# Kernel tuning notes

Hardware: AMD Instinct MI355X
Metric: run time of the kernel (lower is better)

The kernel has to match this reference:

```python
import jax, jax.numpy as jnp
import numpy as np

N_NODES = 100000
N_EDGES = 640000
F_DIM = 128   # node_feature_dim
D_DIM = 128   # state_dim
ROUNDS = 4


def setup_inputs() -> dict:
    key = jax.random.key(0)
    ks = jax.random.split(key, 8)
    s = 1.0 / np.sqrt(D_DIM)
    return {
        "x": jax.random.normal(ks[0], (N_NODES, F_DIM), dtype=jnp.float32),
        "edge_index": jax.random.randint(ks[1], (2, N_EDGES), 0, N_NODES, dtype=jnp.int64),
        "Wi": jax.random.normal(ks[2], (F_DIM, D_DIM), dtype=jnp.float32) * s,
        "bi": jax.random.normal(ks[3], (D_DIM,), dtype=jnp.float32) * s,
        "Wm": jax.random.normal(ks[4], (ROUNDS, D_DIM, D_DIM), dtype=jnp.float32) * s,
        "bm": jax.random.normal(ks[5], (ROUNDS, D_DIM), dtype=jnp.float32) * s,
        "Wu": jax.random.normal(ks[6], (ROUNDS, D_DIM, D_DIM), dtype=jnp.float32) * s,
        "bu": jax.random.normal(ks[7], (ROUNDS, D_DIM), dtype=jnp.float32) * s,
    }


def reference(x, edge_index, Wi, bi, Wm, bm, Wu, bu):
    num_nodes = x.shape[0]
    src = edge_index[0]  # from-node (messages are gathered from here)
    dst = edge_index[1]  # to-node (scatter-add target)

    # input_net: Linear + ReLU
    state = jax.nn.relu(x @ Wi + bi)  # (N, D)

    def step(state, params):
        Wm_r, bm_r, Wu_r, bu_r = params
        message = jax.nn.relu(state @ Wm_r + bm_r)          # (N, D)
        gathered = message[src]                              # (E, D) gather
        aggregated = jax.ops.segment_sum(gathered, dst,
                                         num_segments=num_nodes)  # scatter-add
        return state + jax.nn.relu(aggregated @ Wu_r + bu_r), None

    state, _ = jax.lax.scan(step, state, (Wm, bm, Wu, bu))
    # original: zeros(state_dim) + state broadcasts to (N, D)
    return state
```

## Files before the change

### kernel.cpp

```cpp
#include <hip/hip_runtime.h>

#define NN 100000
#define NE 640000
#define DD 128
#define ROUNDS 4
#define CAP 32
#define NFT 3125
#define GEMMB 512
#define KPH 136

typedef float f32x4 __attribute__((ext_vector_type(4)));
typedef _Float16 half8 __attribute__((ext_vector_type(8)));

__global__ __launch_bounds__(128) void wprep_k(
    const float* __restrict__ Wi, const float* __restrict__ Wm,
    const float* __restrict__ Wu, _Float16* __restrict__ WT)
{
    const int mat = blockIdx.x >> 7;
    const int k   = blockIdx.x & 127;
    const int n   = threadIdx.x;
    const float* W = (mat == 0) ? Wi
                   : (mat <= 4) ? Wm + (size_t)(mat - 1) * DD * DD
                                : Wu + (size_t)(mat - 5) * DD * DD;
    WT[(size_t)mat * DD * DD + (size_t)n * DD + k] = (_Float16)W[(size_t)k * DD + n];
}

__global__ __launch_bounds__(256, 2) void prep_k(
    const float* __restrict__ x,
    const _Float16* __restrict__ WiT, const _Float16* __restrict__ Wm0T,
    const float* __restrict__ bi, const float* __restrict__ bm0,
    _Float16* __restrict__ Sh, _Float16* __restrict__ msg0,
    const int* __restrict__ src, const int* __restrict__ dst,
    int* __restrict__ cursor, int* __restrict__ bucket)
{
    for (int e = blockIdx.x * 256 + threadIdx.x; e < NE; e += GEMMB * 256) {
        const int d = dst[e];
        const int s = src[e];
        const int pos = atomicAdd(&cursor[d], 1);
        if (pos < CAP) bucket[(long long)d * CAP + pos] = s;
    }

    __shared__ _Float16 Ash[32 * KPH];

    const int tid  = threadIdx.x;
    const int lane = tid & 63;
    const int wave = tid >> 6;
    const int ln   = lane & 15;
    const int q    = lane >> 4;
    const int st   = (wave & 1) * 16;
    const int colBase = (wave >> 1) * 64;

    half8 WI[4][4], WM[4][4];
#pragma unroll
    for (int s = 0; s < 4; s++) {
#pragma unroll
        for (int b = 0; b < 4; b++) {
            const size_t off = (size_t)(colBase + b * 16 + ln) * DD + s * 32 + q * 8;
            WI[s][b] = *(const half8*)&WiT[off];
            WM[s][b] = *(const half8*)&Wm0T[off];
        }
    }
    float biasi[4], biasm[4];
#pragma unroll
    for (int b = 0; b < 4; b++) {
        biasi[b] = bi[colBase + b * 16 + ln];
        biasm[b] = bm0[colBase + b * 16 + ln];
    }

    for (int tileB = blockIdx.x; tileB < NFT; tileB += GEMMB) {
        const float* p = x + ((size_t)tileB * 32 + st + ln) * DD + q * 8;
        half8 xa[4];
#pragma unroll
        for (int s = 0; s < 4; s++) {
            const float4 f0 = *(const float4*)&p[s * 32];
            const float4 f1 = *(const float4*)&p[s * 32 + 4];
            half8 h;
            h[0] = (_Float16)f0.x; h[1] = (_Float16)f0.y;
            h[2] = (_Float16)f0.z; h[3] = (_Float16)f0.w;
            h[4] = (_Float16)f1.x; h[5] = (_Float16)f1.y;
            h[6] = (_Float16)f1.z; h[7] = (_Float16)f1.w;
            xa[s] = h;
        }

        f32x4 acc[4];
#pragma unroll
        for (int b = 0; b < 4; b++)
            acc[b] = (f32x4){biasi[b], biasi[b], biasi[b], biasi[b]};
#pragma unroll
        for (int s = 0; s < 4; s++)
#pragma unroll
            for (int b = 0; b < 4; b++)
                acc[b] = __builtin_amdgcn_mfma_f32_16x16x32_f16(xa[s], WI[s][b], acc[b], 0, 0, 0);

        __syncthreads();
#pragma unroll
        for (int b = 0; b < 4; b++) {
            const int col = colBase + b * 16 + ln;
#pragma unroll
            for (int r = 0; r < 4; r++) {
                const size_t row = (size_t)tileB * 32 + st + q * 4 + r;
                const _Float16 v = (_Float16)fmaxf(acc[b][r], 0.f);
                Sh[row * DD + col] = v;
                Ash[(st + q * 4 + r) * KPH + col] = v;
            }
        }
        __syncthreads();

        f32x4 acc2[4];
#pragma unroll
        for (int b = 0; b < 4; b++)
            acc2[b] = (f32x4){biasm[b], biasm[b], biasm[b], biasm[b]};
#pragma unroll
        for (int s = 0; s < 4; s++) {
            const half8 aS = *(const half8*)&Ash[(st + ln) * KPH + s * 32 + q * 8];
#pragma unroll
            for (int b = 0; b < 4; b++)
                acc2[b] = __builtin_amdgcn_mfma_f32_16x16x32_f16(aS, WM[s][b], acc2[b], 0, 0, 0);
        }
#pragma unroll
        for (int b = 0; b < 4; b++) {
            const int col = colBase + b * 16 + ln;
#pragma unroll
            for (int r = 0; r < 4; r++) {
                const size_t row = (size_t)tileB * 32 + st + q * 4 + r;
                msg0[row * DD + col] = (_Float16)fmaxf(acc2[b][r], 0.f);
            }
        }
    }
}

__global__ __launch_bounds__(256, 2) void fused_round_k(
    const _Float16* __restrict__ msgIn,
    const int* __restrict__ cursor,
    const int* __restrict__ bucket,
    const _Float16* __restrict__ WuT, const float* __restrict__ bu_r,
    const _Float16* __restrict__ WmT, const float* __restrict__ bm_r,
    const _Float16* __restrict__ Rh,
    _Float16* __restrict__ ShOut,
    _Float16* __restrict__ msgOut,
    float* __restrict__ Of)
{
    __shared__ _Float16 Ash[32 * KPH];

    const int tid  = threadIdx.x;
    const int lane = tid & 63;
    const int wave = tid >> 6;
    const int ln   = lane & 15;
    const int q    = lane >> 4;
    const int st   = (wave & 1) * 16;
    const int colBase = (wave >> 1) * 64;

    half8 WU[4][4], WM[4][4];
#pragma unroll
    for (int s = 0; s < 4; s++) {
#pragma unroll
        for (int b = 0; b < 4; b++) {
            const size_t off = (size_t)(colBase + b * 16 + ln) * DD + s * 32 + q * 8;
            WU[s][b] = *(const half8*)&WuT[off];
            if (WmT) WM[s][b] = *(const half8*)&WmT[off];
        }
    }
    float biasu[4], biasm[4];
#pragma unroll
    for (int b = 0; b < 4; b++) {
        biasu[b] = bu_r[colBase + b * 16 + ln];
        biasm[b] = WmT ? bm_r[colBase + b * 16 + ln] : 0.f;
    }

    const int grow = tid >> 3;
    const int grp  = tid & 7;
    const int gcol = grp * 16;

    int cnt = 0;
    int idxr[4];
#pragma unroll
    for (int i = 0; i < 4; i++) idxr[i] = 0;
    if (blockIdx.x < NFT) {
        const int node = blockIdx.x * 32 + grow;
        cnt = cursor[node];
        const int ibase = node * CAP;
#pragma unroll
        for (int i = 0; i < 4; i++) idxr[i] = bucket[ibase + grp + 8 * i];
    }

    for (int tileB = blockIdx.x; tileB < NFT; tileB += gridDim.x) {
        const int nextT = tileB + gridDim.x;
        int cntN = 0;
        int idxrN[4];
#pragma unroll
        for (int i = 0; i < 4; i++) idxrN[i] = 0;
        if (nextT < NFT) {
            const int nodeN = nextT * 32 + grow;
            cntN = cursor[nodeN];
            const int ibaseN = nodeN * CAP;
#pragma unroll
            for (int i = 0; i < 4; i++) idxrN[i] = bucket[ibaseN + grp + 8 * i];
        }

        int c = cnt;
        if (c > CAP) c = CAP;

        float a[16];
#pragma unroll
        for (int i = 0; i < 16; i++) a[i] = 0.f;

        for (int j = 0; j < c; j += 4) {
            int ix[4];
#pragma unroll
            for (int u = 0; u < 4; u++) {
                const int jj = (j + u) & 31;
                int v = __shfl(idxr[jj >> 3], (lane & 56) | (jj & 7), 64);
                ix[u] = ((unsigned)v < NN) ? v : 0;
            }
            half8 v[8];
#pragma unroll
            for (int u = 0; u < 4; u++) {
                v[2 * u]     = *(const half8*)&msgIn[(size_t)ix[u] * DD + gcol];
                v[2 * u + 1] = *(const half8*)&msgIn[(size_t)ix[u] * DD + gcol + 8];
            }
#pragma unroll
            for (int u = 0; u < 4; u++) {
                if (j + u < c) {
#pragma unroll
                    for (int i = 0; i < 8; i++) {
                        a[i]     += (float)v[2 * u][i];
                        a[8 + i] += (float)v[2 * u + 1][i];
                    }
                }
            }
        }

        half8 h0, h1;
#pragma unroll
        for (int i = 0; i < 8; i++) { h0[i] = (_Float16)a[i]; h1[i] = (_Float16)a[8 + i]; }

        __syncthreads();
        *(half8*)&Ash[grow * KPH + gcol]     = h0;
        *(half8*)&Ash[grow * KPH + gcol + 8] = h1;
        __syncthreads();

        _Float16 rh[4][4];
#pragma unroll
        for (int b = 0; b < 4; b++)
#pragma unroll
            for (int r = 0; r < 4; r++) {
                const size_t row = (size_t)tileB * 32 + st + q * 4 + r;
                rh[b][r] = Rh[row * DD + colBase + b * 16 + ln];
            }

        f32x4 acc[4];
#pragma unroll
        for (int b = 0; b < 4; b++)
            acc[b] = (f32x4){biasu[b], biasu[b], biasu[b], biasu[b]};
#pragma unroll
        for (int s = 0; s < 4; s++) {
            const half8 aH = *(const half8*)&Ash[(st + ln) * KPH + s * 32 + q * 8];
#pragma unroll
            for (int b = 0; b < 4; b++)
                acc[b] = __builtin_amdgcn_mfma_f32_16x16x32_f16(aH, WU[s][b], acc[b], 0, 0, 0);
        }

        if (!WmT) {
#pragma unroll
            for (int b = 0; b < 4; b++) {
                const int col = colBase + b * 16 + ln;
#pragma unroll
                for (int r = 0; r < 4; r++) {
                    const size_t row = (size_t)tileB * 32 + st + q * 4 + r;
                    Of[row * DD + col] = fmaxf(acc[b][r], 0.f) + (float)rh[b][r];
                }
            }
            cnt = cntN;
#pragma unroll
            for (int i = 0; i < 4; i++) idxr[i] = idxrN[i];
            continue;
        }

        __syncthreads();
#pragma unroll
        for (int b = 0; b < 4; b++) {
            const int col = colBase + b * 16 + ln;
#pragma unroll
            for (int r = 0; r < 4; r++) {
                const size_t row = (size_t)tileB * 32 + st + q * 4 + r;
                const _Float16 v = (_Float16)(fmaxf(acc[b][r], 0.f) + (float)rh[b][r]);
                ShOut[row * DD + col] = v;
                Ash[(st + q * 4 + r) * KPH + col] = v;
            }
        }
        __syncthreads();

        f32x4 acc2[4];
#pragma unroll
        for (int b = 0; b < 4; b++)
            acc2[b] = (f32x4){biasm[b], biasm[b], biasm[b], biasm[b]};
#pragma unroll
        for (int s = 0; s < 4; s++) {
            const half8 aS = *(const half8*)&Ash[(st + ln) * KPH + s * 32 + q * 8];
#pragma unroll
            for (int b = 0; b < 4; b++)
                acc2[b] = __builtin_amdgcn_mfma_f32_16x16x32_f16(aS, WM[s][b], acc2[b], 0, 0, 0);
        }
#pragma unroll
        for (int b = 0; b < 4; b++) {
            const int col = colBase + b * 16 + ln;
#pragma unroll
            for (int r = 0; r < 4; r++) {
                const size_t row = (size_t)tileB * 32 + st + q * 4 + r;
                msgOut[row * DD + col] = (_Float16)fmaxf(acc2[b][r], 0.f);
            }
        }

        cnt = cntN;
#pragma unroll
        for (int i = 0; i < 4; i++) idxr[i] = idxrN[i];
    }
}

extern "C" void kernel_launch(void* const* d_in, const int* in_sizes, int n_in,
                              void* d_out, int out_size, void* d_ws, size_t ws_size,
                              hipStream_t stream) {
    const float* x  = (const float*)d_in[0];
    const int*   ei = (const int*)d_in[1];
    const float* Wi = (const float*)d_in[2];
    const float* bi = (const float*)d_in[3];
    const float* Wm = (const float*)d_in[4];
    const float* bm = (const float*)d_in[5];
    const float* Wu = (const float*)d_in[6];
    const float* bu = (const float*)d_in[7];

    const int* src = ei;
    const int* dst = ei + NE;

    const size_t NELE = (size_t)NN * DD;
    _Float16* msgA = (_Float16*)d_ws;
    _Float16* msgB = msgA + NELE;
    _Float16* Sh   = msgB + NELE;
    _Float16* WT   = Sh + NELE;
    int* cursor = (int*)(WT + 9 * DD * DD);
    int* bucket = cursor + NN;

    hipMemsetAsync(cursor, 0, (size_t)NN * 4, stream);
    wprep_k<<<9 * 128, 128, 0, stream>>>(Wi, Wm, Wu, WT);

    prep_k<<<GEMMB, 256, 0, stream>>>(
        x, WT , WT + 1 * DD * DD , bi, bm,
        Sh, msgA, src, dst, cursor, bucket);

    const int FG = 512;

    _Float16* mIn = msgA;
    _Float16* mOut = msgB;
    for (int r = 0; r < ROUNDS; r++) {
        const bool last = (r == ROUNDS - 1);
        fused_round_k<<<FG, 256, 0, stream>>>(
            mIn, cursor, bucket,
            WT + (size_t)(5 + r) * DD * DD, bu + (size_t)r * DD,
            last ? nullptr : WT + (size_t)(2 + r) * DD * DD,
            last ? nullptr : bm + (size_t)(r + 1) * DD,
            Sh, Sh, mOut,
            last ? (float*)d_out : nullptr);
        _Float16* t = mIn; mIn = mOut; mOut = t;
    }
}
```

Measured before the change: 347.8 us.

## Split fused round into separate gather and GEMM kernels with new wave tiling

Each round's fused gather+GEMM kernel is split into a gather kernel that writes fp16 aggregates to a buffer and a GEMM kernel that reads them back. The GEMM buffer is the same one used for the next message output, processed tile-by-tile in place. Waves now cover 32 columns by all 32 rows instead of 64 by 16, and x is staged through shared memory in prep. Grid sizes and occupancy hints rise. The aim is higher occupancy for the latency-bound gather, at the cost of an extra global round trip of aggregates and twice as many launches.

```diff
diff --git a/kernel.cpp b/kernel.cpp
--- a/kernel.cpp
+++ b/kernel.cpp
@@ -6,7 +6,8 @@
 #define ROUNDS 4
 #define CAP 32
 #define NFT 3125
-#define GEMMB 512
+#define GEMMB 1024
+#define FG 1024
 #define KPH 136
 
 typedef float f32x4 __attribute__((ext_vector_type(4)));
@@ -25,7 +26,7 @@
     WT[(size_t)mat * DD * DD + (size_t)n * DD + k] = (_Float16)W[(size_t)k * DD + n];
 }
 
-__global__ __launch_bounds__(256, 2) void prep_k(
+__global__ __launch_bounds__(256, 3) void prep_k(
     const float* __restrict__ x,
     const _Float16* __restrict__ WiT, const _Float16* __restrict__ Wm0T,
     const float* __restrict__ bi, const float* __restrict__ bm0,
@@ -47,97 +48,178 @@
     const int wave = tid >> 6;
     const int ln   = lane & 15;
     const int q    = lane >> 4;
-    const int st   = (wave & 1) * 16;
-    const int colBase = (wave >> 1) * 64;
-
-    half8 WI[4][4], WM[4][4];
-#pragma unroll
-    for (int s = 0; s < 4; s++) {
-#pragma unroll
-        for (int b = 0; b < 4; b++) {
+    const int colBase = wave * 32;
+
+    half8 WI[4][2], WM[4][2];
+#pragma unroll
+    for (int s = 0; s < 4; s++)
+#pragma unroll
+        for (int b = 0; b < 2; b++) {
             const size_t off = (size_t)(colBase + b * 16 + ln) * DD + s * 32 + q * 8;
             WI[s][b] = *(const half8*)&WiT[off];
             WM[s][b] = *(const half8*)&Wm0T[off];
         }
-    }
-    float biasi[4], biasm[4];
-#pragma unroll
-    for (int b = 0; b < 4; b++) {
+    float biasi[2], biasm[2];
+#pragma unroll
+    for (int b = 0; b < 2; b++) {
         biasi[b] = bi[colBase + b * 16 + ln];
         biasm[b] = bm0[colBase + b * 16 + ln];
     }
 
+    const int grow = tid >> 3;
+    const int grp  = tid & 7;
+    const int gcol = grp * 16;
+
     for (int tileB = blockIdx.x; tileB < NFT; tileB += GEMMB) {
-        const float* p = x + ((size_t)tileB * 32 + st + ln) * DD + q * 8;
-        half8 xa[4];
+        const float* xr = x + ((size_t)tileB * 32 + grow) * DD + gcol;
+        const float4 f0 = *(const float4*)&xr[0];
+        const float4 f1 = *(const float4*)&xr[4];
+        const float4 f2 = *(const float4*)&xr[8];
+        const float4 f3 = *(const float4*)&xr[12];
+        half8 hx0, hx1;
+        hx0[0] = (_Float16)f0.x; hx0[1] = (_Float16)f0.y;
+        hx0[2] = (_Float16)f0.z; hx0[3] = (_Float16)f0.w;
+        hx0[4] = (_Float16)f1.x; hx0[5] = (_Float16)f1.y;
+        hx0[6] = (_Float16)f1.z; hx0[7] = (_Float16)f1.w;
+        hx1[0] = (_Float16)f2.x; hx1[1] = (_Float16)f2.y;
+        hx1[2] = (_Float16)f2.z; hx1[3] = (_Float16)f2.w;
+        hx1[4] = (_Float16)f3.x; hx1[5] = (_Float16)f3.y;
+        hx1[6] = (_Float16)f3.z; hx1[7] = (_Float16)f3.w;
+
+        __syncthreads();
+        *(half8*)&Ash[grow * KPH + gcol]     = hx0;
+        *(half8*)&Ash[grow * KPH + gcol + 8] = hx1;
+        __syncthreads();
+
+        f32x4 acc[2][2];
+#pragma unroll
+        for (int h = 0; h < 2; h++)
+#pragma unroll
+            for (int b = 0; b < 2; b++)
+                acc[h][b] = (f32x4){biasi[b], biasi[b], biasi[b], biasi[b]};
 #pragma unroll
         for (int s = 0; s < 4; s++) {
-            const float4 f0 = *(const float4*)&p[s * 32];
-            const float4 f1 = *(const float4*)&p[s * 32 + 4];
-            half8 h;
-            h[0] = (_Float16)f0.x; h[1] = (_Float16)f0.y;
-            h[2] = (_Float16)f0.z; h[3] = (_Float16)f0.w;
-            h[4] = (_Float16)f1.x; h[5] = (_Float16)f1.y;
-            h[6] = (_Float16)f1.z; h[7] = (_Float16)f1.w;
-            xa[s] = h;
-        }
-
-        f32x4 acc[4];
-#pragma unroll
-        for (int b = 0; b < 4; b++)
-            acc[b] = (f32x4){biasi[b], biasi[b], biasi[b], biasi[b]};
-#pragma unroll
-        for (int s = 0; s < 4; s++)
-#pragma unroll
-            for (int b = 0; b < 4; b++)
-                acc[b] = __builtin_amdgcn_mfma_f32_16x16x32_f16(xa[s], WI[s][b], acc[b], 0, 0, 0);
-
-        __syncthreads();
-#pragma unroll
-        for (int b = 0; b < 4; b++) {
-            const int col = colBase + b * 16 + ln;
-#pragma unroll
-            for (int r = 0; r < 4; r++) {
-                const size_t row = (size_t)tileB * 32 + st + q * 4 + r;
-                const _Float16 v = (_Float16)fmaxf(acc[b][r], 0.f);
-                Sh[row * DD + col] = v;
-                Ash[(st + q * 4 + r) * KPH + col] = v;
-            }
-        }
-        __syncthreads();
-
-        f32x4 acc2[4];
-#pragma unroll
-        for (int b = 0; b < 4; b++)
-            acc2[b] = (f32x4){biasm[b], biasm[b], biasm[b], biasm[b]};
+            const half8 a0 = *(const half8*)&Ash[(ln)      * KPH + s * 32 + q * 8];
+            const half8 a1 = *(const half8*)&Ash[(16 + ln) * KPH + s * 32 + q * 8];
+#pragma unroll
+            for (int b = 0; b < 2; b++) {
+                acc[0][b] = __builtin_amdgcn_mfma_f32_16x16x32_f16(a0, WI[s][b], acc[0][b], 0, 0, 0);
+                acc[1][b] = __builtin_amdgcn_mfma_f32_16x16x32_f16(a1, WI[s][b], acc[1][b], 0, 0, 0);
+            }
+        }
+        __syncthreads();
+
+#pragma unroll
+        for (int h = 0; h < 2; h++)
+#pragma unroll
+            for (int b = 0; b < 2; b++) {
+                const int col = colBase + b * 16 + ln;
+#pragma unroll
+                for (int r = 0; r < 4; r++) {
+                    const int lrow = h * 16 + q * 4 + r;
+                    const size_t row = (size_t)tileB * 32 + lrow;
+                    const _Float16 v = (_Float16)fmaxf(acc[h][b][r], 0.f);
+                    Sh[row * DD + col] = v;
+                    Ash[lrow * KPH + col] = v;
+                }
+            }
+        __syncthreads();
+
+        f32x4 acc2[2][2];
+#pragma unroll
+        for (int h = 0; h < 2; h++)
+#pragma unroll
+            for (int b = 0; b < 2; b++)
+                acc2[h][b] = (f32x4){biasm[b], biasm[b], biasm[b], biasm[b]};
 #pragma unroll
         for (int s = 0; s < 4; s++) {
-            const half8 aS = *(const half8*)&Ash[(st + ln) * KPH + s * 32 + q * 8];
-#pragma unroll
-            for (int b = 0; b < 4; b++)
-                acc2[b] = __builtin_amdgcn_mfma_f32_16x16x32_f16(aS, WM[s][b], acc2[b], 0, 0, 0);
-        }
-#pragma unroll
-        for (int b = 0; b < 4; b++) {
-            const int col = colBase + b * 16 + ln;
-#pragma unroll
-            for (int r = 0; r < 4; r++) {
-                const size_t row = (size_t)tileB * 32 + st + q * 4 + r;
-                msg0[row * DD + col] = (_Float16)fmaxf(acc2[b][r], 0.f);
-            }
-        }
-    }
-}
-
-__global__ __launch_bounds__(256, 2) void fused_round_k(
+            const half8 a0 = *(const half8*)&Ash[(ln)      * KPH + s * 32 + q * 8];
+            const half8 a1 = *(const half8*)&Ash[(16 + ln) * KPH + s * 32 + q * 8];
+#pragma unroll
+            for (int b = 0; b < 2; b++) {
+                acc2[0][b] = __builtin_amdgcn_mfma_f32_16x16x32_f16(a0, WM[s][b], acc2[0][b], 0, 0, 0);
+                acc2[1][b] = __builtin_amdgcn_mfma_f32_16x16x32_f16(a1, WM[s][b], acc2[1][b], 0, 0, 0);
+            }
+        }
+#pragma unroll
+        for (int h = 0; h < 2; h++)
+#pragma unroll
+            for (int b = 0; b < 2; b++) {
+                const int col = colBase + b * 16 + ln;
+#pragma unroll
+                for (int r = 0; r < 4; r++) {
+                    const size_t row = (size_t)tileB * 32 + h * 16 + q * 4 + r;
+                    msg0[row * DD + col] = (_Float16)fmaxf(acc2[h][b][r], 0.f);
+                }
+            }
+    }
+}
+
+__global__ __launch_bounds__(256, 4) void gather_k(
     const _Float16* __restrict__ msgIn,
     const int* __restrict__ cursor,
     const int* __restrict__ bucket,
+    _Float16* __restrict__ agg)
+{
+    const int tid  = threadIdx.x;
+    const int lane = tid & 63;
+    const int grow = tid >> 3;
+    const int grp  = tid & 7;
+    const int gcol = grp * 16;
+
+    const int node = blockIdx.x * 32 + grow;
+    int cnt = cursor[node];
+    if (cnt > CAP) cnt = CAP;
+
+    int idxr[4];
+    const int ibase = node * CAP;
+#pragma unroll
+    for (int i = 0; i < 4; i++) idxr[i] = bucket[ibase + grp + 8 * i];
+
+    float a[16];
+#pragma unroll
+    for (int i = 0; i < 16; i++) a[i] = 0.f;
+
+    for (int j = 0; j < cnt; j += 4) {
+        int ix[4];
+#pragma unroll
+        for (int u = 0; u < 4; u++) {
+            const int jj = (j + u) & 31;
+            int v = __shfl(idxr[jj >> 3], (lane & 56) | (jj & 7), 64);
+            ix[u] = ((unsigned)v < NN) ? v : 0;
+        }
+        half8 v[8];
+#pragma unroll
+        for (int u = 0; u < 4; u++) {
+            v[2 * u]     = *(const half8*)&msgIn[(size_t)ix[u] * DD + gcol];
+            v[2 * u + 1] = *(const half8*)&msgIn[(size_t)ix[u] * DD + gcol + 8];
+        }
+#pragma unroll
+        for (int u = 0; u < 4; u++) {
+            if (j + u < cnt) {
+#pragma unroll
+                for (int i = 0; i < 8; i++) {
+                    a[i]     += (float)v[2 * u][i];
+                    a[8 + i] += (float)v[2 * u + 1][i];
+                }
+            }
+        }
+    }
+
+    half8 h0, h1;
+#pragma unroll
+    for (int i = 0; i < 8; i++) { h0[i] = (_Float16)a[i]; h1[i] = (_Float16)a[8 + i]; }
+    *(half8*)&agg[(size_t)node * DD + gcol]     = h0;
+    *(half8*)&agg[(size_t)node * DD + gcol + 8] = h1;
+}
+
+__global__ __launch_bounds__(256, 3) void gemm_round_k(
+    const _Float16* agg,
     const _Float16* __restrict__ WuT, const float* __restrict__ bu_r,
     const _Float16* __restrict__ WmT, const float* __restrict__ bm_r,
     const _Float16* __restrict__ Rh,
     _Float16* __restrict__ ShOut,
-    _Float16* __restrict__ msgOut,
+    _Float16* msgOut,
     float* __restrict__ Of)
 {
     __shared__ _Float16 Ash[32 * KPH];
@@ -147,22 +229,20 @@
     const int wave = tid >> 6;
     const int ln   = lane & 15;
     const int q    = lane >> 4;
-    const int st   = (wave & 1) * 16;
-    const int colBase = (wave >> 1) * 64;
-
-    half8 WU[4][4], WM[4][4];
-#pragma unroll
-    for (int s = 0; s < 4; s++) {
-#pragma unroll
-        for (int b = 0; b < 4; b++) {
+    const int colBase = wave * 32;
+
+    half8 WU[4][2], WM[4][2];
+#pragma unroll
+    for (int s = 0; s < 4; s++)
+#pragma unroll
+        for (int b = 0; b < 2; b++) {
             const size_t off = (size_t)(colBase + b * 16 + ln) * DD + s * 32 + q * 8;
             WU[s][b] = *(const half8*)&WuT[off];
             if (WmT) WM[s][b] = *(const half8*)&WmT[off];
         }
-    }
-    float biasu[4], biasm[4];
-#pragma unroll
-    for (int b = 0; b < 4; b++) {
+    float biasu[2], biasm[2];
+#pragma unroll
+    for (int b = 0; b < 2; b++) {
         biasu[b] = bu_r[colBase + b * 16 + ln];
         biasm[b] = WmT ? bm_r[colBase + b * 16 + ln] : 0.f;
     }
@@ -171,149 +251,93 @@
     const int grp  = tid & 7;
     const int gcol = grp * 16;
 
-    int cnt = 0;
-    int idxr[4];
-#pragma unroll
-    for (int i = 0; i < 4; i++) idxr[i] = 0;
-    if (blockIdx.x < NFT) {
-        const int node = blockIdx.x * 32 + grow;
-        cnt = cursor[node];
-        const int ibase = node * CAP;
-#pragma unroll
-        for (int i = 0; i < 4; i++) idxr[i] = bucket[ibase + grp + 8 * i];
-    }
-
     for (int tileB = blockIdx.x; tileB < NFT; tileB += gridDim.x) {
-        const int nextT = tileB + gridDim.x;
-        int cntN = 0;
-        int idxrN[4];
-#pragma unroll
-        for (int i = 0; i < 4; i++) idxrN[i] = 0;
-        if (nextT < NFT) {
-            const int nodeN = nextT * 32 + grow;
-            cntN = cursor[nodeN];
-            const int ibaseN = nodeN * CAP;
-#pragma unroll
-            for (int i = 0; i < 4; i++) idxrN[i] = bucket[ibaseN + grp + 8 * i];
-        }
-
-        int c = cnt;
-        if (c > CAP) c = CAP;
-
-        float a[16];
-#pragma unroll
-        for (int i = 0; i < 16; i++) a[i] = 0.f;
-
-        for (int j = 0; j < c; j += 4) {
-            int ix[4];
-#pragma unroll
-            for (int u = 0; u < 4; u++) {
-                const int jj = (j + u) & 31;
-                int v = __shfl(idxr[jj >> 3], (lane & 56) | (jj & 7), 64);
-                ix[u] = ((unsigned)v < NN) ? v : 0;
-            }
-            half8 v[8];
-#pragma unroll
-            for (int u = 0; u < 4; u++) {
-                v[2 * u]     = *(const half8*)&msgIn[(size_t)ix[u] * DD + gcol];
-                v[2 * u + 1] = *(const half8*)&msgIn[(size_t)ix[u] * DD + gcol + 8];
-            }
-#pragma unroll
-            for (int u = 0; u < 4; u++) {
-                if (j + u < c) {
-#pragma unroll
-                    for (int i = 0; i < 8; i++) {
-                        a[i]     += (float)v[2 * u][i];
-                        a[8 + i] += (float)v[2 * u + 1][i];
+        const _Float16* ar = agg + ((size_t)tileB * 32 + grow) * DD + gcol;
+        const half8 g0 = *(const half8*)&ar[0];
+        const half8 g1 = *(const half8*)&ar[8];
+
+        __syncthreads();
+        *(half8*)&Ash[grow * KPH + gcol]     = g0;
+        *(half8*)&Ash[grow * KPH + gcol + 8] = g1;
+        __syncthreads();
+
+        f32x4 acc[2][2];
+#pragma unroll
+        for (int h = 0; h < 2; h++)
+#pragma unroll
+            for (int b = 0; b < 2; b++)
+                acc[h][b] = (f32x4){biasu[b], biasu[b], biasu[b], biasu[b]};
+#pragma unroll
+        for (int s = 0; s < 4; s++) {
+            const half8 a0 = *(const half8*)&Ash[(ln)      * KPH + s * 32 + q * 8];
+            const half8 a1 = *(const half8*)&Ash[(16 + ln) * KPH + s * 32 + q * 8];
+#pragma unroll
+            for (int b = 0; b < 2; b++) {
+                acc[0][b] = __builtin_amdgcn_mfma_f32_16x16x32_f16(a0, WU[s][b], acc[0][b], 0, 0, 0);
+                acc[1][b] = __builtin_amdgcn_mfma_f32_16x16x32_f16(a1, WU[s][b], acc[1][b], 0, 0, 0);
+            }
+        }
+
+        if (!WmT) {
+#pragma unroll
+            for (int h = 0; h < 2; h++)
+#pragma unroll
+                for (int b = 0; b < 2; b++) {
+                    const int col = colBase + b * 16 + ln;
+#pragma unroll
+                    for (int r = 0; r < 4; r++) {
+                        const size_t row = (size_t)tileB * 32 + h * 16 + q * 4 + r;
+                        Of[row * DD + col] = fmaxf(acc[h][b][r], 0.f) + (float)Rh[row * DD + col];
                     }
                 }
-            }
-        }
-
-        half8 h0, h1;
-#pragma unroll
-        for (int i = 0; i < 8; i++) { h0[i] = (_Float16)a[i]; h1[i] = (_Float16)a[8 + i]; }
-
-        __syncthreads();
-        *(half8*)&Ash[grow * KPH + gcol]     = h0;
-        *(half8*)&Ash[grow * KPH + gcol + 8] = h1;
-        __syncthreads();
-
-        _Float16 rh[4][4];
-#pragma unroll
-        for (int b = 0; b < 4; b++)
-#pragma unroll
-            for (int r = 0; r < 4; r++) {
-                const size_t row = (size_t)tileB * 32 + st + q * 4 + r;
-                rh[b][r] = Rh[row * DD + colBase + b * 16 + ln];
-            }
-
-        f32x4 acc[4];
-#pragma unroll
-        for (int b = 0; b < 4; b++)
-            acc[b] = (f32x4){biasu[b], biasu[b], biasu[b], biasu[b]};
+            continue;
+        }
+
+        __syncthreads();
+#pragma unroll
+        for (int h = 0; h < 2; h++)
+#pragma unroll
+            for (int b = 0; b < 2; b++) {
+                const int col = colBase + b * 16 + ln;
+#pragma unroll
+                for (int r = 0; r < 4; r++) {
+                    const int lrow = h * 16 + q * 4 + r;
+                    const size_t row = (size_t)tileB * 32 + lrow;
+                    const _Float16 v =
+                        (_Float16)(fmaxf(acc[h][b][r], 0.f) + (float)Rh[row * DD + col]);
+                    ShOut[row * DD + col] = v;
+                    Ash[lrow * KPH + col] = v;
+                }
+            }
+        __syncthreads();
+
+        f32x4 acc2[2][2];
+#pragma unroll
+        for (int h = 0; h < 2; h++)
+#pragma unroll
+            for (int b = 0; b < 2; b++)
+                acc2[h][b] = (f32x4){biasm[b], biasm[b], biasm[b], biasm[b]};
 #pragma unroll
         for (int s = 0; s < 4; s++) {
-            const half8 aH = *(const half8*)&Ash[(st + ln) * KPH + s * 32 + q * 8];
-#pragma unroll
-            for (int b = 0; b < 4; b++)
-                acc[b] = __builtin_amdgcn_mfma_f32_16x16x32_f16(aH, WU[s][b], acc[b], 0, 0, 0);
-        }
-
-        if (!WmT) {
-#pragma unroll
-            for (int b = 0; b < 4; b++) {
+            const half8 a0 = *(const half8*)&Ash[(ln)      * KPH + s * 32 + q * 8];
+            const half8 a1 = *(const half8*)&Ash[(16 + ln) * KPH + s * 32 + q * 8];
+#pragma unroll
+            for (int b = 0; b < 2; b++) {
+                acc2[0][b] = __builtin_amdgcn_mfma_f32_16x16x32_f16(a0, WM[s][b], acc2[0][b], 0, 0, 0);
+                acc2[1][b] = __builtin_amdgcn_mfma_f32_16x16x32_f16(a1, WM[s][b], acc2[1][b], 0, 0, 0);
+            }
+        }
+#pragma unroll
+        for (int h = 0; h < 2; h++)
+#pragma unroll
+            for (int b = 0; b < 2; b++) {
                 const int col = colBase + b * 16 + ln;
 #pragma unroll
                 for (int r = 0; r < 4; r++) {
-                    const size_t row = (size_t)tileB * 32 + st + q * 4 + r;
-                    Of[row * DD + col] = fmaxf(acc[b][r], 0.f) + (float)rh[b][r];
-                }
-            }
-            cnt = cntN;
-#pragma unroll
-            for (int i = 0; i < 4; i++) idxr[i] = idxrN[i];
-            continue;
-        }
-
-        __syncthreads();
-#pragma unroll
-        for (int b = 0; b < 4; b++) {
-            const int col = colBase + b * 16 + ln;
-#pragma unroll
-            for (int r = 0; r < 4; r++) {
-                const size_t row = (size_t)tileB * 32 + st + q * 4 + r;
-                const _Float16 v = (_Float16)(fmaxf(acc[b][r], 0.f) + (float)rh[b][r]);
-                ShOut[row * DD + col] = v;
-                Ash[(st + q * 4 + r) * KPH + col] = v;
-            }
-        }
-        __syncthreads();
-
-        f32x4 acc2[4];
-#pragma unroll
-        for (int b = 0; b < 4; b++)
-            acc2[b] = (f32x4){biasm[b], biasm[b], biasm[b], biasm[b]};
-#pragma unroll
-        for (int s = 0; s < 4; s++) {
-            const half8 aS = *(const half8*)&Ash[(st + ln) * KPH + s * 32 + q * 8];
-#pragma unroll
-            for (int b = 0; b < 4; b++)
-                acc2[b] = __builtin_amdgcn_mfma_f32_16x16x32_f16(aS, WM[s][b], acc2[b], 0, 0, 0);
-        }
-#pragma unroll
-        for (int b = 0; b < 4; b++) {
-            const int col = colBase + b * 16 + ln;
-#pragma unroll
-            for (int r = 0; r < 4; r++) {
-                const size_t row = (size_t)tileB * 32 + st + q * 4 + r;
-                msgOut[row * DD + col] = (_Float16)fmaxf(acc2[b][r], 0.f);
-            }
-        }
-
-        cnt = cntN;
-#pragma unroll
-        for (int i = 0; i < 4; i++) idxr[i] = idxrN[i];
+                    const size_t row = (size_t)tileB * 32 + h * 16 + q * 4 + r;
+                    msgOut[row * DD + col] = (_Float16)fmaxf(acc2[h][b][r], 0.f);
+                }
+            }
     }
 }
 
@@ -347,18 +371,18 @@
         x, WT , WT + 1 * DD * DD , bi, bm,
         Sh, msgA, src, dst, cursor, bucket);
 
-    const int FG = 512;
-
     _Float16* mIn = msgA;
     _Float16* mOut = msgB;
     for (int r = 0; r < ROUNDS; r++) {
         const bool last = (r == ROUNDS - 1);
-        fused_round_k<<<FG, 256, 0, stream>>>(
-            mIn, cursor, bucket,
+        gather_k<<<NFT, 256, 0, stream>>>(mIn, cursor, bucket, mOut);
+        gemm_round_k<<<FG, 256, 0, stream>>>(
+            mOut ,
             WT + (size_t)(5 + r) * DD * DD, bu + (size_t)r * DD,
             last ? nullptr : WT + (size_t)(2 + r) * DD * DD,
             last ? nullptr : bm + (size_t)(r + 1) * DD,
-            Sh, Sh, mOut,
+            Sh, Sh,
+            mOut ,
             last ? (float*)d_out : nullptr);
         _Float16* t = mIn; mIn = mOut; mOut = t;
     }
```

Result: slower. 434.7 us (+25.0%).
